# Performance work log

Measured on AMD Instinct MI355X. Metric: run time of the kernel, lower is better.

## Reference

```python
import jax, jax.numpy as jnp
import numpy as np
import math

NQ = 8            # n_qubits (hardcoded in _TransformerBlockQuantum)
DIM = 2 ** NQ     # statevector size = 256
H = 16            # num_heads
EPS = 1e-5        # LayerNorm eps

# PauliZ expectation table: wire 0 = most significant bit. ZTAB[w, j] = +/-1
_bits = (np.arange(DIM)[None, :] >> (NQ - 1 - np.arange(NQ)[:, None])) & 1
ZTAB = (1.0 - 2.0 * _bits).astype(np.float32)  # [NQ, DIM]


def _apply_1q(state, gate, w):
    # state: [N, 2^NQ] complex, gate: [N, 2, 2] complex, acts on wire w (MSB ordering)
    N = state.shape[0]
    s = state.reshape(N, 2 ** w, 2, 2 ** (NQ - w - 1))
    s = jnp.einsum('nab,npbq->npaq', gate, s)
    return s.reshape(N, DIM)


def _apply_cnot(state, c):
    # CNOT with control wire c, target wire c+1 (adjacent chain)
    N = state.shape[0]
    s = state.reshape(N, 2 ** c, 2, 2, 2 ** (NQ - c - 2))
    s = jnp.concatenate([s[:, :, :1], jnp.flip(s[:, :, 1:], axis=3)], axis=2)
    return s.reshape(N, DIM)


def _layernorm(x, g, b):
    mu = jnp.mean(x, axis=-1, keepdims=True)
    var = jnp.mean((x - mu) ** 2, axis=-1, keepdims=True)
    return (x - mu) / jnp.sqrt(var + EPS) * g + b


def _quantum_ffn(x, Win, b_in, Wout, b_out, ry):
    B, S, D = x.shape
    ang = (jnp.einsum('bsd,qd->bsq', x, Win) + b_in).reshape(-1, NQ)  # [N, NQ]
    N = ang.shape[0]
    state = jnp.zeros((N, DIM), jnp.complex64).at[:, 0].set(1.0)
    # RX encoding (per-token angles)
    for w in range(NQ):
        th = ang[:, w] * 0.5
        c, s = jnp.cos(th), jnp.sin(th)
        g = jnp.stack([jnp.stack([c, -1j * s], -1), jnp.stack([-1j * s, c], -1)], -2)
        state = _apply_1q(state, g.astype(jnp.complex64), w)
    # trainable RY (shared angles)
    for w in range(NQ):
        th = ry[w] * 0.5
        c, s = jnp.cos(th), jnp.sin(th)
        g = jnp.stack([jnp.stack([c, -s]), jnp.stack([s, c])]).astype(jnp.complex64)
        state = _apply_1q(state, jnp.broadcast_to(g, (N, 2, 2)), w)
    # CNOT entangling chain
    for w in range(NQ - 1):
        state = _apply_cnot(state, w)
    probs = jnp.abs(state) ** 2                      # [N, DIM] float32
    expz = probs @ ZTAB.T                            # [N, NQ]
    out = jnp.einsum('bsq,dq->bsd', expz.reshape(B, S, NQ), Wout) + b_out
    return jax.nn.relu(out)  # dropout = identity in eval


def _forward(x, Wq, Wk, Wv, Wo, g1, b1, g2, b2, Win, b_in, Wout, b_out, ry):
    B, S, D = x.shape
    dk = D // H
    q = jnp.einsum('bsd,ed->bse', x, Wq).reshape(B, S, H, dk)
    k = jnp.einsum('bsd,ed->bse', x, Wk).reshape(B, S, H, dk)
    v = jnp.einsum('bsd,ed->bse', x, Wv).reshape(B, S, H, dk)
    scores = jnp.einsum('bqhd,bkhd->bhqk', q, k) / math.sqrt(dk)
    attn = jax.nn.softmax(scores, axis=-1)
    o = jnp.einsum('bhqk,bkhd->bqhd', attn, v).reshape(B, S, D)
    attn_out = jnp.einsum('bsd,ed->bse', o, Wo)
    x1 = _layernorm(x + attn_out, g1, b1)
    ffn_out = _quantum_ffn(x1, Win, b_in, Wout, b_out, ry)
    return _layernorm(x1 + ffn_out, g2, b2)


def setup_inputs() -> dict:
    key = jax.random.key(0)
    ks = jax.random.split(key, 16)
    B, S, D = 2, 2048, 1024
    sd = 1.0 / math.sqrt(D)
    return {
        'x': jax.random.normal(ks[0], (B, S, D), jnp.float32),
        'Wq': jax.random.normal(ks[1], (D, D), jnp.float32) * sd,
        'Wk': jax.random.normal(ks[2], (D, D), jnp.float32) * sd,
        'Wv': jax.random.normal(ks[3], (D, D), jnp.float32) * sd,
        'Wo': jax.random.normal(ks[4], (D, D), jnp.float32) * sd,
        'g1': jnp.ones((D,), jnp.float32),
        'b1': jnp.zeros((D,), jnp.float32),
        'g2': jnp.ones((D,), jnp.float32),
        'b2': jnp.zeros((D,), jnp.float32),
        'Win': jax.random.normal(ks[5], (NQ, D), jnp.float32) * sd,
        'b_in': jnp.zeros((NQ,), jnp.float32),
        'Wout': jax.random.normal(ks[6], (D, NQ), jnp.float32) * (1.0 / math.sqrt(NQ)),
        'b_out': jnp.zeros((D,), jnp.float32),
        'ry': jax.random.normal(ks[7], (NQ,), jnp.float32) * 0.1,
    }


def reference(x, Wq, Wk, Wv, Wo, g1, b1, g2, b2, Win, b_in, Wout, b_out, ry):
    return _forward(x, Wq, Wk, Wv, Wo, g1, b1, g2, b2, Win, b_in, Wout, b_out, ry)
```

## Files before the change

kernel.cpp:

```cpp
#include <hip/hip_runtime.h>
#include <stdint.h>


typedef unsigned short u16;
typedef unsigned int   u32;
typedef __bf16 bf16x8 __attribute__((ext_vector_type(8)));
typedef u16    u16x8  __attribute__((ext_vector_type(8)));
typedef u16    u16x4  __attribute__((ext_vector_type(4)));
typedef float  f32x4  __attribute__((ext_vector_type(4)));
typedef float  f32x16 __attribute__((ext_vector_type(16)));

#define DEV static __device__ __forceinline__

DEV u16 f2b(float f){ u32 u = __float_as_uint(f); return (u16)((u + 0x7fffu + ((u>>16)&1u)) >> 16); }
DEV u16 b2u(__bf16 h){ union{__bf16 b; u16 u;} c; c.b = h; return c.u; }
DEV float exp2fast(float x){ return __builtin_amdgcn_exp2f(x); }

DEV void plswap(u32 a, u32 b, u32& o0, u32& o1, int hi){
#if __has_builtin(__builtin_amdgcn_permlane32_swap)
  auto s = __builtin_amdgcn_permlane32_swap(a, b, false, false);
  o0 = s[0]; o1 = s[1];
#else
  u32 xa = __shfl_xor(a, 32), xb = __shfl_xor(b, 32);
  o0 = hi ? xb : a;
  o1 = hi ? b  : xa;
#endif
}

#define MFMA16(a,b,c) __builtin_amdgcn_mfma_f32_16x16x32_bf16((a),(b),(c),0,0,0)
#define MFMA32(a,b,c) __builtin_amdgcn_mfma_f32_32x32x16_bf16((a),(b),(c),0,0,0)
#define GLD16(gp,lp) __builtin_amdgcn_global_load_lds( \
    (const __attribute__((address_space(1))) u32*)(const void*)(gp), \
    (__attribute__((address_space(3))) u32*)(void*)(lp), 16, 0, 0)

__global__ __launch_bounds__(256) void k_cast(const float* __restrict__ src, u16* __restrict__ dst){
  const int i = blockIdx.x*256 + threadIdx.x;
  const f32x4* s = (const f32x4*)src + (size_t)i*2;
  f32x4 a = s[0], b = s[1];
  u16x8 o;
  o[0]=f2b(a.x); o[1]=f2b(a.y); o[2]=f2b(a.z); o[3]=f2b(a.w);
  o[4]=f2b(b.x); o[5]=f2b(b.y); o[6]=f2b(b.z); o[7]=f2b(b.w);
  ((u16x8*)dst)[i] = o;
}

__global__ __launch_bounds__(256) void k_cast_w(
    const float* __restrict__ Wq, const float* __restrict__ Wk,
    const float* __restrict__ Wv, const float* __restrict__ Wo,
    u16* __restrict__ wb, u16* __restrict__ wob){
  const int r = blockIdx.x >> 9, bi = blockIdx.x & 511;
  const float* src = (r==0)?Wq:((r==1)?Wk:((r==2)?Wv:Wo));
  u16* dst = (r<3) ? (wb + (size_t)r*1048576) : wob;
  const int i = bi*256 + threadIdx.x;
  const f32x4* s = (const f32x4*)src + (size_t)i*2;
  f32x4 a = s[0], b = s[1];
  u16x8 o;
  o[0]=f2b(a.x); o[1]=f2b(a.y); o[2]=f2b(a.z); o[3]=f2b(a.w);
  o[4]=f2b(b.x); o[5]=f2b(b.y); o[6]=f2b(b.z); o[7]=f2b(b.w);
  ((u16x8*)dst)[i] = o;
}

template<int MODE>
__global__ __launch_bounds__(256) void k_gemm_nt(
    const u16* __restrict__ A, const u16* __restrict__ B,
    float* __restrict__ Cf, u16* __restrict__ Qo, u16* __restrict__ Ko, u16* __restrict__ Vt,
    int K, int N)
{
  __shared__ __attribute__((aligned(16))) u16 As[128*64];
  __shared__ __attribute__((aligned(16))) u16 Bs[128*64];
  const int tid = threadIdx.x, lane = tid & 63, w = tid >> 6;
  const int wr = w >> 1, wc = w & 1;
  const int nwg = gridDim.x * gridDim.y;
  int lin = blockIdx.y * gridDim.x + blockIdx.x;
  lin = (lin & 7) * (nwg >> 3) + (lin >> 3);
  const int n0 = (lin % gridDim.x) * 128;
  const int m0 = (lin / gridDim.x) * 128;
  const int l15 = lane & 15, lg = lane >> 4;
  f32x4 acc[4][4] = {};
  const int lr = lane >> 3, lc = (lane & 7)*8;
  const u16* ag = A + (size_t)(m0 + w*32 + lr)*K + lc;
  const u16* bg = B + (size_t)(n0 + w*32 + lr)*K + lc;
  u16* asl = &As[(w*32)*64];
  u16* bsl = &Bs[(w*32)*64];
  for (int k0 = 0; k0 < K; k0 += 64){
    __syncthreads();
    #pragma unroll
    for (int c = 0; c < 4; ++c){
      GLD16(ag + (size_t)(c*8)*K + k0, asl + c*512);
      GLD16(bg + (size_t)(c*8)*K + k0, bsl + c*512);
    }
    __syncthreads();
    #pragma unroll
    for (int kk = 0; kk < 2; ++kk){
      const int ko = kk*32 + lg*8;
      bf16x8 af[4], bf[4];
      #pragma unroll
      for (int t=0;t<4;++t) af[t] = *(const bf16x8*)&As[(wr*64 + t*16 + l15)*64 + ko];
      #pragma unroll
      for (int t=0;t<4;++t) bf[t] = *(const bf16x8*)&Bs[(wc*64 + t*16 + l15)*64 + ko];
      #pragma unroll
      for (int i=0;i<4;++i)
        #pragma unroll
        for (int j=0;j<4;++j)
          acc[i][j] = MFMA16(af[i], bf[j], acc[i][j]);
    }
  }
  const int col0 = n0 + wc*64 + l15;
  const int row0 = m0 + wr*64 + lg*4;
  if (MODE==0){
    const int which = n0 >> 10;
    if (which == 2){
      #pragma unroll
      for (int i=0;i<4;++i){
        const int rr0 = row0 + i*16;
        const int bsel = rr0 >> 11, ss = rr0 & 2047;
        #pragma unroll
        for (int j=0;j<4;++j){
          const int d_loc = (col0 + j*16) & 1023;
          const int hh = d_loc >> 6, dd = d_loc & 63;
          u16x4 pk;
          #pragma unroll
          for (int r=0;r<4;++r) pk[r] = f2b(acc[i][j][r]);
          *(u16x4*)(Vt + ((size_t)((bsel*16 + hh)*64 + dd))*2048 + ss) = pk;
        }
      }
    } else {
      u16* dst = which ? Ko : Qo;
      const float scl = which ? 1.f : 0.125f*1.44269504f;
      #pragma unroll
      for (int i=0;i<4;++i)
      #pragma unroll
      for (int j=0;j<4;++j){
        const int cc = (col0 + j*16) & 1023;
        #pragma unroll
        for (int r=0;r<4;++r)
          dst[(size_t)(row0 + i*16 + r)*1024 + cc] = f2b(acc[i][j][r]*scl);
      }
    }
  } else {
    #pragma unroll
    for (int i=0;i<4;++i)
    #pragma unroll
    for (int j=0;j<4;++j){
      const int cc = col0 + j*16;
      #pragma unroll
      for (int r=0;r<4;++r)
        Cf[(size_t)(row0 + i*16 + r)*N + cc] = acc[i][j][r];
    }
  }
}

__global__ __launch_bounds__(256) void k_attn(
    const u16* __restrict__ q, const u16* __restrict__ k,
    const u16* __restrict__ vt, u16* __restrict__ o)
{
  __shared__ __attribute__((aligned(16))) char KVb[2][16384];
  const int tid = threadIdx.x, lane = tid & 63, w = tid >> 6;
  const int p = blockIdx.x >> 4, qt = blockIdx.x & 15;
  const int b = p >> 4, h = p & 15;
  const int l31 = lane & 31, hi = lane >> 5;
  const int qrow = b*2048 + qt*128 + w*32 + l31;
  const int swz = (l31 & 7) << 4;
  bf16x8 qa[4];
  #pragma unroll
  for (int kk=0;kk<4;++kk)
    qa[kk] = *(const bf16x8*)(q + (size_t)qrow*1024 + h*64 + kk*16 + hi*8);
  const char* kgl[2]; const char* vgl[2]; int ldsK[2], ldsV[2];
  #pragma unroll
  for (int i=0;i<2;++i){
    const int s = w*2048 + i*1024 + lane*16;
    const int row = s >> 7;
    const int cb = (s & 127) ^ ((row & 7) << 4);
    kgl[i] = (const char*)k  + ((size_t)(b*2048 + row))*2048 + h*128 + cb;
    vgl[i] = (const char*)vt + ((size_t)(p*64    + row))*4096 + cb;
    ldsK[i] = w*2048 + i*1024;
    ldsV[i] = 8192 + w*2048 + i*1024;
  }
  f32x16 oacc[2] = {};
  float mrow = -1e30f, lrow = 0.f;
  int cur = 0;
  #pragma unroll
  for (int i=0;i<2;++i){ GLD16(kgl[i], KVb[0] + ldsK[i]); GLD16(vgl[i], KVb[0] + ldsV[i]); }
  for (int it = 0; it < 32; ++it){
    __syncthreads();
    if (it < 31){
      const size_t nkv = (size_t)(it+1)*64;
      #pragma unroll
      for (int i=0;i<2;++i){
        GLD16(kgl[i] + nkv*2048, KVb[cur^1] + ldsK[i]);
        GLD16(vgl[i] + nkv*2,    KVb[cur^1] + ldsV[i]);
      }
    }
    const char* Kb = KVb[cur];
    const char* Vb = KVb[cur] + 8192;
    f32x16 sacc[2] = {};
    __builtin_amdgcn_s_setprio(1);
    #pragma unroll
    for (int t32=0;t32<2;++t32){
      const int row = t32*32 + l31;
      #pragma unroll
      for (int kk=0;kk<4;++kk){
        bf16x8 kf = *(const bf16x8*)(Kb + row*128 + ((kk*32 + hi*16) ^ swz));
        sacc[t32] = MFMA32(kf, qa[kk], sacc[t32]);
      }
    }
    __builtin_amdgcn_s_setprio(0);
    float mx = sacc[0][0];
    #pragma unroll
    for (int t32=0;t32<2;++t32)
      #pragma unroll
      for (int i=0;i<16;++i) mx = fmaxf(mx, sacc[t32][i]);
    mx = fmaxf(mx, __shfl_xor(mx, 32));
    if (!__all(mx <= mrow + 8.f)){
      const float mnew = fmaxf(mrow, mx);
      const float scl = exp2fast(mrow - mnew);
      mrow = mnew; lrow *= scl;
      #pragma unroll
      for (int dt=0;dt<2;++dt)
        #pragma unroll
        for (int i=0;i<16;++i) oacc[dt][i] *= scl;
    }
    float rsum = 0.f;
    #pragma unroll
    for (int t32=0;t32<2;++t32)
      #pragma unroll
      for (int i=0;i<16;++i){
        const float e = exp2fast(sacc[t32][i] - mrow);
        sacc[t32][i] = e; rsum += e;
      }
    rsum += __shfl_xor(rsum, 32);
    lrow += rsum;
    u32 pk[2][8];
    #pragma unroll
    for (int t32=0;t32<2;++t32)
      #pragma unroll
      for (int u=0;u<8;++u){
        const int idx = (u>>1)*4 + (u&1)*2;
        const u32 lo = b2u((__bf16)sacc[t32][idx]);
        const u32 hh = b2u((__bf16)sacc[t32][idx+1]);
        pk[t32][u] = lo | (hh << 16);
      }
    bf16x8 pb[4];
    #pragma unroll
    for (int op=0;op<4;++op){
      const int t32 = op>>1, base = (op&1)*4;
      u32 w0,w1,w2,w3;
      plswap(pk[t32][base+0], pk[t32][base+2], w0, w2, hi);
      plswap(pk[t32][base+1], pk[t32][base+3], w1, w3, hi);
      union { u32 u[4]; bf16x8 v; } cc;
      cc.u[0]=w0; cc.u[1]=w1; cc.u[2]=w2; cc.u[3]=w3;
      pb[op] = cc.v;
    }
    __builtin_amdgcn_s_setprio(1);
    #pragma unroll
    for (int dt=0;dt<2;++dt){
      const int row = dt*32 + l31;
      #pragma unroll
      for (int op=0;op<4;++op){
        bf16x8 vf = *(const bf16x8*)(Vb + row*128 + ((op*32 + hi*16) ^ swz));
        oacc[dt] = MFMA32(vf, pb[op], oacc[dt]);
      }
    }
    __builtin_amdgcn_s_setprio(0);
    cur ^= 1;
  }
  const float rinv = 1.f / lrow;
  u16* orow = o + (size_t)qrow*1024 + h*64;
  #pragma unroll
  for (int dt=0;dt<2;++dt)
    #pragma unroll
    for (int rg=0;rg<4;++rg)
      #pragma unroll
      for (int hf=0;hf<2;++hf){
        const int r0 = rg*4 + hf*2;
        const u32 lo = b2u((__bf16)(oacc[dt][r0]   * rinv));
        const u32 hh = b2u((__bf16)(oacc[dt][r0+1] * rinv));
        *(u32*)(orow + dt*32 + rg*8 + hi*4 + hf*2) = lo | (hh << 16);
      }
}

__global__ __launch_bounds__(256) void k_tail(
    const float* __restrict__ x, const float* __restrict__ attn,
    const float* __restrict__ g1, const float* __restrict__ b1,
    const float* __restrict__ Win, const float* __restrict__ b_in,
    const float* __restrict__ Wout, const float* __restrict__ b_out,
    const float* __restrict__ ry,
    const float* __restrict__ g2, const float* __restrict__ b2,
    float* __restrict__ out)
{
  const int tid = threadIdx.x, lane = tid & 63, w = tid >> 6;
  const int t = blockIdx.x*4 + w;
  const size_t base = (size_t)t*1024;
  f32x4 yv[4];
  float s1 = 0.f, s2 = 0.f;
  #pragma unroll
  for (int c=0;c<4;++c){
    const int idx = c*256 + lane*4;
    f32x4 xv = *(const f32x4*)(x + base + idx);
    f32x4 av = *(const f32x4*)(attn + base + idx);
    f32x4 y = xv + av;
    yv[c] = y;
    s1 += y.x + y.y + y.z + y.w;
    s2 += y.x*y.x + y.y*y.y + y.z*y.z + y.w*y.w;
  }
  #pragma unroll
  for (int off=32; off; off>>=1){ s1 += __shfl_xor(s1, off); s2 += __shfl_xor(s2, off); }
  {
    const float mu = s1*(1.f/1024.f);
    const float rinv = rsqrtf(s2*(1.f/1024.f) - mu*mu + 1e-5f);
    #pragma unroll
    for (int c=0;c<4;++c){
      const int idx = c*256 + lane*4;
      f32x4 gv = *(const f32x4*)(g1 + idx);
      f32x4 bv = *(const f32x4*)(b1 + idx);
      f32x4 y = yv[c];
      y.x = (y.x-mu)*rinv*gv.x + bv.x;
      y.y = (y.y-mu)*rinv*gv.y + bv.y;
      y.z = (y.z-mu)*rinv*gv.z + bv.z;
      y.w = (y.w-mu)*rinv*gv.w + bv.w;
      yv[c] = y;
    }
  }
  float ang[8];
  #pragma unroll
  for (int qq=0; qq<8; ++qq){
    float acc = 0.f;
    #pragma unroll
    for (int c=0;c<4;++c){
      f32x4 wv = *(const f32x4*)(Win + qq*1024 + c*256 + lane*4);
      acc += wv.x*yv[c].x + wv.y*yv[c].y + wv.z*yv[c].z + wv.w*yv[c].w;
    }
    ang[qq] = acc;
  }
  #pragma unroll
  for (int off=32; off; off>>=1)
    #pragma unroll
    for (int qq=0; qq<8; ++qq) ang[qq] += __shfl_xor(ang[qq], off);
  #pragma unroll
  for (int qq=0; qq<8; ++qq) ang[qq] += b_in[qq];
  float vr[4], vi[4];
  #pragma unroll
  for (int r=0;r<4;++r){ vr[r]=0.f; vi[r]=0.f; }
  if (lane==0) vr[0] = 1.f;
  #pragma unroll
  for (int wi=0; wi<8; ++wi){
    float s, c; __sincosf(ang[wi]*0.5f, &s, &c);
    const int pbit = 7 - wi;
    if (pbit >= 6){
      const int rp = 1 << (pbit-6);
      #pragma unroll
      for (int r=0;r<4;++r) if (!(r & rp)){
        const int r2 = r | rp;
        float ar=vr[r], ai=vi[r], br=vr[r2], bi=vi[r2];
        vr[r]  = c*ar + s*bi;  vi[r]  = c*ai - s*br;
        vr[r2] = c*br + s*ai;  vi[r2] = c*bi - s*ar;
      }
    } else {
      const int msk = 1 << pbit;
      #pragma unroll
      for (int r=0;r<4;++r){
        float orr = __shfl_xor(vr[r], msk);
        float oii = __shfl_xor(vi[r], msk);
        float nr = c*vr[r] + s*oii;
        float ni = c*vi[r] - s*orr;
        vr[r]=nr; vi[r]=ni;
      }
    }
  }
  #pragma unroll
  for (int wi=0; wi<8; ++wi){
    float s, c; __sincosf(ry[wi]*0.5f, &s, &c);
    const int pbit = 7 - wi;
    if (pbit >= 6){
      const int rp = 1 << (pbit-6);
      #pragma unroll
      for (int r=0;r<4;++r) if (!(r & rp)){
        const int r2 = r | rp;
        float ar=vr[r], ai=vi[r], br=vr[r2], bi=vi[r2];
        vr[r]  = c*ar - s*br;  vi[r]  = c*ai - s*bi;
        vr[r2] = s*ar + c*br;  vi[r2] = s*ai + c*bi;
      }
    } else {
      const int msk = 1 << pbit;
      const float sg = (lane & msk) ? s : -s;
      #pragma unroll
      for (int r=0;r<4;++r){
        float orr = __shfl_xor(vr[r], msk);
        float oii = __shfl_xor(vi[r], msk);
        float nr = c*vr[r] + sg*orr;
        float ni = c*vi[r] + sg*oii;
        vr[r]=nr; vi[r]=ni;
      }
    }
  }
  { float tr=vr[2]; vr[2]=vr[3]; vr[3]=tr; float ti=vi[2]; vi[2]=vi[3]; vi[3]=ti; }
  vr[1]=__shfl_xor(vr[1],32); vi[1]=__shfl_xor(vi[1],32);
  vr[3]=__shfl_xor(vr[3],32); vi[3]=__shfl_xor(vi[3],32);
  #pragma unroll
  for (int cn=2; cn<7; ++cn){
    const int pc = 7-cn, pt = pc-1;
    const bool ctl = (lane >> pc) & 1;
    #pragma unroll
    for (int r=0;r<4;++r){
      float tr = __shfl_xor(vr[r], 1<<pt);
      float ti = __shfl_xor(vi[r], 1<<pt);
      if (ctl){ vr[r]=tr; vi[r]=ti; }
    }
  }
  float pr[4];
  #pragma unroll
  for (int r=0;r<4;++r) pr[r] = vr[r]*vr[r] + vi[r]*vi[r];
  float e[8];
  e[0] = (pr[0]+pr[1]) - (pr[2]+pr[3]);
  e[1] = (pr[0]+pr[2]) - (pr[1]+pr[3]);
  const float tot = pr[0]+pr[1]+pr[2]+pr[3];
  #pragma unroll
  for (int wi=2; wi<8; ++wi){
    const int pbit = 7-wi;
    e[wi] = ((lane >> pbit) & 1) ? -tot : tot;
  }
  #pragma unroll
  for (int off=1; off<64; off<<=1)
    #pragma unroll
    for (int i=0;i<8;++i) e[i] += __shfl_xor(e[i], off);
  float yy[4][4];
  s1 = 0.f; s2 = 0.f;
  #pragma unroll
  for (int c=0;c<4;++c){
    const float x1a[4] = {yv[c].x, yv[c].y, yv[c].z, yv[c].w};
    #pragma unroll
    for (int j=0;j<4;++j){
      const int d = c*256 + lane*4 + j;
      f32x4 w0 = *(const f32x4*)(Wout + (size_t)d*8);
      f32x4 w1 = *(const f32x4*)(Wout + (size_t)d*8 + 4);
      float acc = b_out[d];
      acc += w0.x*e[0] + w0.y*e[1] + w0.z*e[2] + w0.w*e[3];
      acc += w1.x*e[4] + w1.y*e[5] + w1.z*e[6] + w1.w*e[7];
      const float y = x1a[j] + fmaxf(acc, 0.f);
      yy[c][j] = y;
      s1 += y; s2 += y*y;
    }
  }
  #pragma unroll
  for (int off=32; off; off>>=1){ s1 += __shfl_xor(s1, off); s2 += __shfl_xor(s2, off); }
  const float mu = s1*(1.f/1024.f);
  const float rinv = rsqrtf(s2*(1.f/1024.f) - mu*mu + 1e-5f);
  #pragma unroll
  for (int c=0;c<4;++c){
    const int idx = c*256 + lane*4;
    f32x4 gv = *(const f32x4*)(g2 + idx);
    f32x4 bv = *(const f32x4*)(b2 + idx);
    f32x4 ov;
    ov.x = (yy[c][0]-mu)*rinv*gv.x + bv.x;
    ov.y = (yy[c][1]-mu)*rinv*gv.y + bv.y;
    ov.z = (yy[c][2]-mu)*rinv*gv.z + bv.z;
    ov.w = (yy[c][3]-mu)*rinv*gv.w + bv.w;
    *(f32x4*)(out + base + idx) = ov;
  }
}

extern "C" void kernel_launch(void* const* d_in, const int* in_sizes, int n_in,
                              void* d_out, int out_size, void* d_ws, size_t ws_size,
                              hipStream_t stream)
{
  const float* x    = (const float*)d_in[0];
  const float* Wq   = (const float*)d_in[1];
  const float* Wk   = (const float*)d_in[2];
  const float* Wv   = (const float*)d_in[3];
  const float* Wo   = (const float*)d_in[4];
  const float* g1   = (const float*)d_in[5];
  const float* b1   = (const float*)d_in[6];
  const float* g2   = (const float*)d_in[7];
  const float* b2   = (const float*)d_in[8];
  const float* Win  = (const float*)d_in[9];
  const float* b_in = (const float*)d_in[10];
  const float* Wout = (const float*)d_in[11];
  const float* b_out= (const float*)d_in[12];
  const float* ry   = (const float*)d_in[13];
  float* out = (float*)d_out;
  char* ws = (char*)d_ws;
  const size_t MB = 1024u*1024u;
  u16* xb  = (u16*)(ws + 0*MB);
  u16* wb  = (u16*)(ws + 8*MB);
  u16* wob = (u16*)(ws + 14*MB);
  u16* qb  = (u16*)(ws + 16*MB);
  u16* kb  = (u16*)(ws + 24*MB);
  u16* vtb = (u16*)(ws + 32*MB);
  u16* ob  = (u16*)(ws + 40*MB);
  float* attn_out = (float*)(ws + 48*MB);

  k_cast<<<2048, 256, 0, stream>>>(x, xb);
  k_cast_w<<<2048, 256, 0, stream>>>(Wq, Wk, Wv, Wo, wb, wob);
  k_gemm_nt<0><<<dim3(24,32), 256, 0, stream>>>(xb, wb, nullptr, qb, kb, vtb, 1024, 3072);
  k_attn<<<512, 256, 0, stream>>>(qb, kb, vtb, ob);
  k_gemm_nt<1><<<dim3(8,32), 256, 0, stream>>>(ob, wob, attn_out, nullptr, nullptr, nullptr, 1024, 1024);
  k_tail<<<1024, 256, 0, stream>>>(x, attn_out, g1, b1, Win, b_in, Wout, b_out, ry, g2, b2, out);
}
```

Measured before the change: 268.9 us.

## Split attention KV range across two wave groups with LDS merge

Each attention block now runs 512 threads, split into two groups of four waves. Each group processes half of the key/value sequence (16 iterations instead of 32) with its own double-buffered LDS region. At the end, group 1 writes its partial output (as bf16) and its max/sum statistics to LDS, and group 0 merges them with its own using a log-sum-exp rescale. The aim is more parallelism per query tile and shorter serial KV loops, since there are only 512 blocks. The costs are 64KB of LDS per block, which may limit occupancy, an extra merge step, and bf16 rounding of the partial accumulator.

```diff
diff --git a/kernel.cpp b/kernel.cpp
--- a/kernel.cpp
+++ b/kernel.cpp
@@ -149,49 +149,52 @@
   }
 }
 
-__global__ __launch_bounds__(256) void k_attn(
+__global__ __launch_bounds__(512) void k_attn(
     const u16* __restrict__ q, const u16* __restrict__ k,
     const u16* __restrict__ vt, u16* __restrict__ o)
 {
-  __shared__ __attribute__((aligned(16))) char KVb[2][16384];
-  const int tid = threadIdx.x, lane = tid & 63, w = tid >> 6;
+  __shared__ __attribute__((aligned(16))) char KVb[65536];
+  const int tid = threadIdx.x, lane = tid & 63;
+  const int wl = (tid >> 6) & 3, wg = tid >> 8;
   const int p = blockIdx.x >> 4, qt = blockIdx.x & 15;
   const int b = p >> 4, h = p & 15;
   const int l31 = lane & 31, hi = lane >> 5;
-  const int qrow = b*2048 + qt*128 + w*32 + l31;
+  const int qrow = b*2048 + qt*128 + wl*32 + l31;
   const int swz = (l31 & 7) << 4;
   bf16x8 qa[4];
   #pragma unroll
   for (int kk=0;kk<4;++kk)
     qa[kk] = *(const bf16x8*)(q + (size_t)qrow*1024 + h*64 + kk*16 + hi*8);
-  const char* kgl[2]; const char* vgl[2]; int ldsK[2], ldsV[2];
+  const char* kgl[2]; const char* vgl[2];
   #pragma unroll
   for (int i=0;i<2;++i){
-    const int s = w*2048 + i*1024 + lane*16;
+    const int s = wl*2048 + i*1024 + lane*16;
     const int row = s >> 7;
     const int cb = (s & 127) ^ ((row & 7) << 4);
-    kgl[i] = (const char*)k  + ((size_t)(b*2048 + row))*2048 + h*128 + cb;
-    vgl[i] = (const char*)vt + ((size_t)(p*64    + row))*4096 + cb;
-    ldsK[i] = w*2048 + i*1024;
-    ldsV[i] = 8192 + w*2048 + i*1024;
-  }
+    kgl[i] = (const char*)k  + ((size_t)(b*2048 + wg*1024 + row))*2048 + h*128 + cb;
+    vgl[i] = (const char*)vt + ((size_t)(p*64 + row))*4096 + wg*2048 + cb;
+  }
+  const int gbase = wg*32768;
   f32x16 oacc[2] = {};
   float mrow = -1e30f, lrow = 0.f;
-  int cur = 0;
-  #pragma unroll
-  for (int i=0;i<2;++i){ GLD16(kgl[i], KVb[0] + ldsK[i]); GLD16(vgl[i], KVb[0] + ldsV[i]); }
-  for (int it = 0; it < 32; ++it){
+  #pragma unroll
+  for (int i=0;i<2;++i){
+    GLD16(kgl[i], KVb + gbase + wl*2048 + i*1024);
+    GLD16(vgl[i], KVb + gbase + 8192 + wl*2048 + i*1024);
+  }
+  for (int it = 0; it < 16; ++it){
     __syncthreads();
-    if (it < 31){
+    if (it < 15){
       const size_t nkv = (size_t)(it+1)*64;
+      const int nb = gbase + (((it+1)&1)<<14);
       #pragma unroll
       for (int i=0;i<2;++i){
-        GLD16(kgl[i] + nkv*2048, KVb[cur^1] + ldsK[i]);
-        GLD16(vgl[i] + nkv*2,    KVb[cur^1] + ldsV[i]);
-      }
-    }
-    const char* Kb = KVb[cur];
-    const char* Vb = KVb[cur] + 8192;
+        GLD16(kgl[i] + nkv*2048, KVb + nb + wl*2048 + i*1024);
+        GLD16(vgl[i] + nkv*2,    KVb + nb + 8192 + wl*2048 + i*1024);
+      }
+    }
+    const char* Kb = KVb + gbase + ((it&1)<<14);
+    const char* Vb = Kb + 8192;
     f32x16 sacc[2] = {};
     __builtin_amdgcn_s_setprio(1);
     #pragma unroll
@@ -261,21 +264,50 @@
       }
     }
     __builtin_amdgcn_s_setprio(0);
-    cur ^= 1;
-  }
-  const float rinv = 1.f / lrow;
-  u16* orow = o + (size_t)qrow*1024 + h*64;
-  #pragma unroll
-  for (int dt=0;dt<2;++dt)
+  }
+  __syncthreads();
+  char* OB = KVb + 32768;
+  char* MLB = KVb + 49152;
+  if (wg == 1){
+    #pragma unroll
+    for (int dt=0;dt<2;++dt)
     #pragma unroll
     for (int rg=0;rg<4;++rg)
-      #pragma unroll
-      for (int hf=0;hf<2;++hf){
-        const int r0 = rg*4 + hf*2;
-        const u32 lo = b2u((__bf16)(oacc[dt][r0]   * rinv));
-        const u32 hh = b2u((__bf16)(oacc[dt][r0+1] * rinv));
-        *(u32*)(orow + dt*32 + rg*8 + hi*4 + hf*2) = lo | (hh << 16);
-      }
+    #pragma unroll
+    for (int hf=0;hf<2;++hf){
+      const int r0 = rg*4 + hf*2;
+      const u32 lo = b2u((__bf16)oacc[dt][r0]);
+      const u32 hh = b2u((__bf16)oacc[dt][r0+1]);
+      const int j = dt*8 + rg*2 + hf;
+      *(u32*)(OB + wl*4096 + j*256 + lane*4) = lo | (hh << 16);
+    }
+    if (hi == 0)
+      *(float2*)(MLB + (wl*32 + l31)*8) = make_float2(mrow, lrow);
+  }
+  __syncthreads();
+  if (wg == 0){
+    const float2 ml1 = *(const float2*)(MLB + (wl*32 + l31)*8);
+    const float m  = fmaxf(mrow, ml1.x);
+    const float a0 = exp2fast(mrow - m), a1 = exp2fast(ml1.x - m);
+    const float linv = 1.f / (lrow*a0 + ml1.y*a1);
+    const float s0 = a0*linv, s1 = a1*linv;
+    u16* orow = o + (size_t)qrow*1024 + h*64;
+    #pragma unroll
+    for (int dt=0;dt<2;++dt)
+    #pragma unroll
+    for (int rg=0;rg<4;++rg)
+    #pragma unroll
+    for (int hf=0;hf<2;++hf){
+      const int r0 = rg*4 + hf*2;
+      const int j = dt*8 + rg*2 + hf;
+      const u32 pu = *(const u32*)(OB + wl*4096 + j*256 + lane*4);
+      const float p0 = __uint_as_float(pu << 16);
+      const float p1 = __uint_as_float(pu & 0xFFFF0000u);
+      const float v0 = oacc[dt][r0]  *s0 + p0*s1;
+      const float v1 = oacc[dt][r0+1]*s0 + p1*s1;
+      *(u32*)(orow + dt*32 + rg*8 + hi*4 + hf*2) = (u32)b2u((__bf16)v0) | ((u32)b2u((__bf16)v1) << 16);
+    }
+  }
 }
 
 __global__ __launch_bounds__(256) void k_tail(
@@ -491,7 +523,7 @@
   k_cast<<<2048, 256, 0, stream>>>(x, xb);
   k_cast_w<<<2048, 256, 0, stream>>>(Wq, Wk, Wv, Wo, wb, wob);
   k_gemm_nt<0><<<dim3(24,32), 256, 0, stream>>>(xb, wb, nullptr, qb, kb, vtb, 1024, 3072);
-  k_attn<<<512, 256, 0, stream>>>(qb, kb, vtb, ob);
+  k_attn<<<512, 512, 0, stream>>>(qb, kb, vtb, ob);
   k_gemm_nt<1><<<dim3(8,32), 256, 0, stream>>>(ob, wob, attn_out, nullptr, nullptr, nullptr, 1024, 1024);
   k_tail<<<1024, 256, 0, stream>>>(x, attn_out, g1, b1, Win, b_in, Wout, b_out, ry, g2, b2, out);
 }
```

Result: no change. 266.4 us (-0.9%).

## Give each attention wave private KV double buffers and drop block barriers

Applied to the files above, without the earlier changes.

Each wave now stages its own K/V tiles into a private 16KB slice of shared memory, with 32-key steps and a per-wave double buffer, so the loop no longer needs __syncthreads. Ordering is handled with explicit vmcnt waits. The intent is to stop the four waves from waiting on each other and to overlap loads with compute per wave. The cost is that each K/V tile is now loaded from global memory four times, once per wave, which raises global traffic. Shared memory grows to 64KB per block, and launch bounds now request 2 blocks per CU.

```diff
diff --git a/kernel.cpp b/kernel.cpp
--- a/kernel.cpp
+++ b/kernel.cpp
@@ -149,66 +149,67 @@
   }
 }
 
-__global__ __launch_bounds__(256) void k_attn(
+__global__ __launch_bounds__(256, 2) void k_attn(
     const u16* __restrict__ q, const u16* __restrict__ k,
     const u16* __restrict__ vt, u16* __restrict__ o)
 {
-  __shared__ __attribute__((aligned(16))) char KVb[2][16384];
-  const int tid = threadIdx.x, lane = tid & 63, w = tid >> 6;
+  __shared__ __attribute__((aligned(16))) char WS[65536];
+  const int tid = threadIdx.x, lane = tid & 63, wl = tid >> 6;
   const int p = blockIdx.x >> 4, qt = blockIdx.x & 15;
   const int b = p >> 4, h = p & 15;
   const int l31 = lane & 31, hi = lane >> 5;
-  const int qrow = b*2048 + qt*128 + w*32 + l31;
-  const int swz = (l31 & 7) << 4;
+  const int qrow = b*2048 + qt*128 + wl*32 + l31;
   bf16x8 qa[4];
   #pragma unroll
   for (int kk=0;kk<4;++kk)
     qa[kk] = *(const bf16x8*)(q + (size_t)qrow*1024 + h*64 + kk*16 + hi*8);
-  const char* kgl[2]; const char* vgl[2]; int ldsK[2], ldsV[2];
-  #pragma unroll
-  for (int i=0;i<2;++i){
-    const int s = w*2048 + i*1024 + lane*16;
-    const int row = s >> 7;
-    const int cb = (s & 127) ^ ((row & 7) << 4);
-    kgl[i] = (const char*)k  + ((size_t)(b*2048 + row))*2048 + h*128 + cb;
-    vgl[i] = (const char*)vt + ((size_t)(p*64    + row))*4096 + cb;
-    ldsK[i] = w*2048 + i*1024;
-    ldsV[i] = 8192 + w*2048 + i*1024;
-  }
+  const char* kgl[4]; const char* vgl[4];
+  #pragma unroll
+  for (int c=0;c<4;++c){
+    const int rowK = c*8 + (lane >> 3);
+    const int cbK  = ((lane & 7)*16) ^ ((rowK & 7) << 4);
+    kgl[c] = (const char*)k + ((size_t)(b*2048 + rowK))*2048 + h*128 + cbK;
+    const int rowV = c*16 + (lane >> 2);
+    const int cbV  = ((lane & 3)*16) ^ ((rowV & 3) << 4);
+    vgl[c] = (const char*)vt + ((size_t)(p*64 + rowV))*4096 + cbV;
+  }
+  char* wbase = WS + wl*16384;
+  #pragma unroll
+  for (int c=0;c<4;++c){ GLD16(kgl[c], wbase + c*1024); GLD16(vgl[c], wbase + 4096 + c*1024); }
   f32x16 oacc[2] = {};
   float mrow = -1e30f, lrow = 0.f;
-  int cur = 0;
-  #pragma unroll
-  for (int i=0;i<2;++i){ GLD16(kgl[i], KVb[0] + ldsK[i]); GLD16(vgl[i], KVb[0] + ldsV[i]); }
-  for (int it = 0; it < 32; ++it){
-    __syncthreads();
-    if (it < 31){
-      const size_t nkv = (size_t)(it+1)*64;
-      #pragma unroll
-      for (int i=0;i<2;++i){
-        GLD16(kgl[i] + nkv*2048, KVb[cur^1] + ldsK[i]);
-        GLD16(vgl[i] + nkv*2,    KVb[cur^1] + ldsV[i]);
-      }
-    }
-    const char* Kb = KVb[cur];
-    const char* Vb = KVb[cur] + 8192;
-    f32x16 sacc[2] = {};
+  const int kswz = (l31 & 7) << 4, vswz = (l31 & 3) << 4;
+  for (int it = 0; it < 64; ++it){
+    char* db = wbase + ((it & 1) << 13);
+    if (it < 63){
+      char* nb = wbase + (((it+1) & 1) << 13);
+      const size_t ko = (size_t)(it+1)*65536;
+      const int    vo = (it+1)*64;
+      #pragma unroll
+      for (int c=0;c<4;++c){ GLD16(kgl[c] + ko, nb + c*1024); GLD16(vgl[c] + vo, nb + 4096 + c*1024); }
+      asm volatile("s_waitcnt vmcnt(8)" ::: "memory");
+    } else {
+      asm volatile("s_waitcnt vmcnt(0)" ::: "memory");
+    }
+    __builtin_amdgcn_sched_barrier(0);
+    bf16x8 kf[4];
+    #pragma unroll
+    for (int kk=0;kk<4;++kk)
+      kf[kk] = *(const bf16x8*)(db + l31*128 + ((kk*32 + hi*16) ^ kswz));
+    f32x16 sacc = {};
     __builtin_amdgcn_s_setprio(1);
     #pragma unroll
-    for (int t32=0;t32<2;++t32){
-      const int row = t32*32 + l31;
-      #pragma unroll
-      for (int kk=0;kk<4;++kk){
-        bf16x8 kf = *(const bf16x8*)(Kb + row*128 + ((kk*32 + hi*16) ^ swz));
-        sacc[t32] = MFMA32(kf, qa[kk], sacc[t32]);
-      }
-    }
+    for (int kk=0;kk<4;++kk) sacc = MFMA32(kf[kk], qa[kk], sacc);
     __builtin_amdgcn_s_setprio(0);
-    float mx = sacc[0][0];
-    #pragma unroll
-    for (int t32=0;t32<2;++t32)
-      #pragma unroll
-      for (int i=0;i<16;++i) mx = fmaxf(mx, sacc[t32][i]);
+    bf16x8 vf[2][2];
+    #pragma unroll
+    for (int dt=0;dt<2;++dt)
+      #pragma unroll
+      for (int op=0;op<2;++op)
+        vf[dt][op] = *(const bf16x8*)(db + 4096 + (dt*32 + l31)*64 + ((op*32 + hi*16) ^ vswz));
+    float mx = sacc[0];
+    #pragma unroll
+    for (int i=1;i<16;++i) mx = fmaxf(mx, sacc[i]);
     mx = fmaxf(mx, __shfl_xor(mx, 32));
     if (!__all(mx <= mrow + 8.f)){
       const float mnew = fmaxf(mrow, mx);
@@ -221,47 +222,36 @@
     }
     float rsum = 0.f;
     #pragma unroll
-    for (int t32=0;t32<2;++t32)
-      #pragma unroll
-      for (int i=0;i<16;++i){
-        const float e = exp2fast(sacc[t32][i] - mrow);
-        sacc[t32][i] = e; rsum += e;
-      }
+    for (int i=0;i<16;++i){
+      const float e = exp2fast(sacc[i] - mrow);
+      sacc[i] = e; rsum += e;
+    }
     rsum += __shfl_xor(rsum, 32);
     lrow += rsum;
-    u32 pk[2][8];
-    #pragma unroll
-    for (int t32=0;t32<2;++t32)
-      #pragma unroll
-      for (int u=0;u<8;++u){
-        const int idx = (u>>1)*4 + (u&1)*2;
-        const u32 lo = b2u((__bf16)sacc[t32][idx]);
-        const u32 hh = b2u((__bf16)sacc[t32][idx+1]);
-        pk[t32][u] = lo | (hh << 16);
-      }
-    bf16x8 pb[4];
-    #pragma unroll
-    for (int op=0;op<4;++op){
-      const int t32 = op>>1, base = (op&1)*4;
+    u32 pk[8];
+    #pragma unroll
+    for (int u=0;u<8;++u){
+      const int idx = (u>>1)*4 + (u&1)*2;
+      pk[u] = (u32)b2u((__bf16)sacc[idx]) | ((u32)b2u((__bf16)sacc[idx+1]) << 16);
+    }
+    bf16x8 pb[2];
+    #pragma unroll
+    for (int op=0;op<2;++op){
+      const int base = op*4;
       u32 w0,w1,w2,w3;
-      plswap(pk[t32][base+0], pk[t32][base+2], w0, w2, hi);
-      plswap(pk[t32][base+1], pk[t32][base+3], w1, w3, hi);
+      plswap(pk[base+0], pk[base+2], w0, w2, hi);
+      plswap(pk[base+1], pk[base+3], w1, w3, hi);
       union { u32 u[4]; bf16x8 v; } cc;
       cc.u[0]=w0; cc.u[1]=w1; cc.u[2]=w2; cc.u[3]=w3;
       pb[op] = cc.v;
     }
     __builtin_amdgcn_s_setprio(1);
     #pragma unroll
-    for (int dt=0;dt<2;++dt){
-      const int row = dt*32 + l31;
-      #pragma unroll
-      for (int op=0;op<4;++op){
-        bf16x8 vf = *(const bf16x8*)(Vb + row*128 + ((op*32 + hi*16) ^ swz));
-        oacc[dt] = MFMA32(vf, pb[op], oacc[dt]);
-      }
-    }
+    for (int dt=0;dt<2;++dt)
+      #pragma unroll
+      for (int op=0;op<2;++op)
+        oacc[dt] = MFMA32(vf[dt][op], pb[op], oacc[dt]);
     __builtin_amdgcn_s_setprio(0);
-    cur ^= 1;
   }
   const float rinv = 1.f / lrow;
   u16* orow = o + (size_t)qrow*1024 + h*64;
```

Measured after the change: 279.0 us. +3.7%, slower.
